# Optimization experiments

Measured on AMD Instinct MI355X. Metric: run time of the kernel, lower is better.

The kernel has to match this reference:

```python
import jax, jax.numpy as jnp
import numpy as np

N, E, DIN, HID, HEADS = 50000, 400000, 256, 64, 4
EPS_BN = 1e-5

def setup_inputs() -> dict:
    key = jax.random.key(0)
    ks = jax.random.split(key, 12)
    inp = {}
    inp['x'] = jax.random.normal(ks[0], (N, DIN), dtype=jnp.float32)
    inp['edge_index'] = jax.random.randint(ks[1], (2, E), 0, N, dtype=jnp.int64)
    s = 1.0 / np.sqrt(DIN)
    inp['W1'] = jax.random.uniform(ks[2], (DIN, HEADS * HID), jnp.float32, -s, s)
    inp['a_src1'] = jax.random.normal(ks[3], (HEADS, HID), dtype=jnp.float32) * 0.1
    inp['a_dst1'] = jax.random.normal(ks[4], (HEADS, HID), dtype=jnp.float32) * 0.1
    inp['b1'] = jnp.zeros((HEADS * HID,), jnp.float32)
    inp['bn1_w'] = jnp.ones((HEADS * HID,), jnp.float32)
    inp['bn1_b'] = jnp.zeros((HEADS * HID,), jnp.float32)
    inp['bn1_m'] = jnp.zeros((HEADS * HID,), jnp.float32)
    inp['bn1_v'] = jnp.ones((HEADS * HID,), jnp.float32)
    s2 = 1.0 / np.sqrt(HEADS * HID)
    inp['W2'] = jax.random.uniform(ks[5], (HEADS * HID, HID), jnp.float32, -s2, s2)
    inp['a_src2'] = jax.random.normal(ks[6], (1, HID), dtype=jnp.float32) * 0.1
    inp['a_dst2'] = jax.random.normal(ks[7], (1, HID), dtype=jnp.float32) * 0.1
    inp['b2'] = jnp.zeros((HID,), jnp.float32)
    inp['bn2_w'] = jnp.ones((HID,), jnp.float32)
    inp['bn2_b'] = jnp.zeros((HID,), jnp.float32)
    inp['bn2_m'] = jnp.zeros((HID,), jnp.float32)
    inp['bn2_v'] = jnp.ones((HID,), jnp.float32)
    sr = 1.0 / np.sqrt(HID)
    inp['Wr'] = jax.random.uniform(ks[8], (HID, 1), jnp.float32, -sr, sr)
    inp['br'] = jnp.zeros((1,), jnp.float32)
    inp['Wc'] = jax.random.uniform(ks[9], (HID, 1), jnp.float32, -sr, sr)
    inp['bc'] = jnp.zeros((1,), jnp.float32)
    return inp

def gat_layer(x, src, dst, W, a_src, a_dst, bias, concat):
    # x: [N, Fin] -> h: [N, H, D]
    H, D = a_src.shape
    h = (x @ W).reshape(-1, H, D)
    alpha_s = jnp.sum(h * a_src[None], axis=-1)  # [N, H]
    alpha_d = jnp.sum(h * a_dst[None], axis=-1)
    e = jax.nn.leaky_relu(alpha_s[src] + alpha_d[dst], 0.2)  # [Et, H]
    m = jax.ops.segment_max(e, dst, num_segments=N)
    m = jnp.where(jnp.isfinite(m), m, 0.0)
    ex = jnp.exp(e - m[dst])
    denom = jax.ops.segment_sum(ex, dst, num_segments=N)
    alpha = ex / (denom[dst] + 1e-16)  # segment softmax over incoming edges
    msg = h[src] * alpha[:, :, None]  # [Et, H, D]
    out = jax.ops.segment_sum(msg, dst, num_segments=N)  # [N, H, D]
    out = out.reshape(N, H * D) if concat else out.mean(axis=1)
    return out + bias

def batchnorm(x, w, b, mean, var):
    return (x - mean) * jax.lax.rsqrt(var + EPS_BN) * w + b

def reference(x, edge_index, W1, a_src1, a_dst1, b1, bn1_w, bn1_b, bn1_m, bn1_v,
              W2, a_src2, a_dst2, b2, bn2_w, bn2_b, bn2_m, bn2_v, Wr, br, Wc, bc):
    # add self loops (PyG GATConv default)
    loops = jnp.arange(N, dtype=edge_index.dtype)
    src = jnp.concatenate([edge_index[0], loops])
    dst = jnp.concatenate([edge_index[1], loops])
    h = gat_layer(x, src, dst, W1, a_src1, a_dst1, b1, concat=True)
    h = jax.nn.elu(batchnorm(h, bn1_w, bn1_b, bn1_m, bn1_v))
    h = gat_layer(h, src, dst, W2, a_src2, a_dst2, b2, concat=False)
    h = jax.nn.elu(batchnorm(h, bn2_w, bn2_b, bn2_m, bn2_v))
    reg = h @ Wr + br
    clf = jax.nn.sigmoid(h @ Wc + bc)
    return reg, clf
```

## Files before the change

kernel.cpp:

```cpp
#include <hip/hip_runtime.h>
#include <math.h>


typedef unsigned short ushort_t;
typedef unsigned char uchar_t;
typedef __attribute__((ext_vector_type(8))) unsigned short ushort8;
typedef __attribute__((ext_vector_type(4))) unsigned short ushort4v;
typedef __attribute__((ext_vector_type(8))) short short8;
typedef __attribute__((ext_vector_type(4))) float f32x4;
typedef __attribute__((ext_vector_type(2))) float f32x2;

#define EPS_BN 1e-5f

__device__ __forceinline__ ushort_t f2bf(float f) {
  unsigned u = __float_as_uint(f);
  unsigned r = u + 0x7fffu + ((u >> 16) & 1u);
  return (ushort_t)(r >> 16);
}
__device__ __forceinline__ float bf2f(ushort_t h) {
  return __uint_as_float((unsigned)h << 16);
}
__device__ __forceinline__ uchar_t f2fp8(float f) {
  return (uchar_t)(__builtin_amdgcn_cvt_pk_fp8_f32(f, f, 0, false) & 0xff);
}
__device__ __forceinline__ float leaky02(float x) { return x >= 0.f ? x : 0.2f * x; }
__device__ __forceinline__ float elu_fast(float x) {
  return x > 0.f ? x : __expf(x) - 1.f;
}
__device__ __forceinline__ float wave_sum(float v) {
#pragma unroll
  for (int o = 1; o < 64; o <<= 1) v += __shfl_xor(v, o, 64);
  return v;
}
__device__ __forceinline__ int wave_incl_scan(int v, int lane) {
#pragma unroll
  for (int off = 1; off < 64; off <<= 1) {
    int t = __shfl_up(v, off, 64);
    if (lane >= off) v += t;
  }
  return v;
}

__device__ __forceinline__ void gld_lds16(const ushort_t* g, ushort_t* l) {
  __builtin_amdgcn_global_load_lds(
      (const __attribute__((address_space(1))) unsigned int*)g,
      (__attribute__((address_space(3))) unsigned int*)l, 16, 0, 0);
}

__global__ __launch_bounds__(256) void hist_kernel(
    const int* __restrict__ dst, int* __restrict__ counts, int E) {
  int e = blockIdx.x * blockDim.x + threadIdx.x;
  if (e < E) atomicAdd(&counts[dst[e]], 1);
}

__global__ __launch_bounds__(256) void scan_chunks_kernel(
    const int* __restrict__ counts, int* __restrict__ offsets, int* __restrict__ partials,
    int N, int E, int* __restrict__ csr_src,
    const float* __restrict__ W1, const float* __restrict__ W2,
    ushort_t* __restrict__ W1t, ushort_t* __restrict__ W2t,
    const float* __restrict__ b1, const float* __restrict__ bn1w,
    const float* __restrict__ bn1b, const float* __restrict__ bn1m,
    const float* __restrict__ bn1v,
    const float* __restrict__ b2, const float* __restrict__ bn2w,
    const float* __restrict__ bn2b, const float* __restrict__ bn2m,
    const float* __restrict__ bn2v,
    float* __restrict__ S1, float* __restrict__ T1,
    float* __restrict__ S2, float* __restrict__ T2) {
  __shared__ int ws[4];
  const int tid = threadIdx.x, lane = tid & 63, wv = tid >> 6;
  const int i = blockIdx.x * 256 + tid;
  const int gsz = gridDim.x * 256;
  int v = (i < N) ? counts[i] : 0;
  int incl = wave_incl_scan(v, lane);
  if (lane == 63) ws[wv] = incl;
  __syncthreads();
  int wbase = 0;
  for (int k = 0; k < wv; ++k) wbase += ws[k];
  if (i < N) offsets[i] = wbase + incl - v;
  if (tid == 255) partials[blockIdx.x] = wbase + incl;

  for (int j = i; j < 256 * 256; j += gsz) {
    int k = j >> 8, n2 = j & 255;
    W1t[n2 * 256 + k] = f2bf(W1[j]);
  }
  for (int j = i; j < 256 * 64; j += gsz) {
    int k = j >> 6, n2 = j & 63;
    W2t[n2 * 256 + k] = f2bf(W2[j]);
  }
  if (i < 256) {
    float s = bn1w[i] * rsqrtf(bn1v[i] + EPS_BN);
    S1[i] = s;
    T1[i] = (b1[i] - bn1m[i]) * s + bn1b[i];
  } else if (i < 320) {
    int j = i - 256;
    float s = bn2w[j] * rsqrtf(bn2v[j] + EPS_BN);
    S2[j] = s;
    T2[j] = (b2[j] - bn2m[j]) * s + bn2b[j];
  } else if (i < 384) {
    csr_src[E + i - 320] = 0;
  }
}

__global__ __launch_bounds__(256) void scatter_kernel(
    const int* __restrict__ src, const int* __restrict__ dst,
    const int* __restrict__ offsets, const int* __restrict__ partials,
    int* __restrict__ cursor, int* __restrict__ csr_src,
    int* __restrict__ offs2, int E, int N, int nb) {
  __shared__ int pp[256];
  __shared__ int ws[4];
  __shared__ int tot;
  const int tid = threadIdx.x, lane = tid & 63, wv = tid >> 6;
  int v = (tid < nb) ? partials[tid] : 0;
  int incl = wave_incl_scan(v, lane);
  if (lane == 63) ws[wv] = incl;
  __syncthreads();
  int wbase = 0;
  for (int k = 0; k < wv; ++k) wbase += ws[k];
  pp[tid] = wbase + incl - v;
  if (tid == 255) tot = wbase + incl;
  __syncthreads();

  int idx = blockIdx.x * 256 + tid;
  if (idx < E) {
    int d = dst[idx];
    int p = atomicAdd(&cursor[d], 1);
    csr_src[offsets[d] + pp[d >> 8] + p] = src[idx];
  }
  if (idx <= N) {
    offs2[idx] = (idx < N) ? offsets[idx] + pp[idx >> 8] : tot;
  }
}

__global__ __launch_bounds__(512) void gemm1_persist(
    const float* __restrict__ X, const ushort_t* __restrict__ Bt,
    uchar_t* __restrict__ Cout, const float* __restrict__ avs,
    const float* __restrict__ avd,
    float* __restrict__ as_out, float* __restrict__ ad_out, int M, int ntiles) {
  __shared__ ushort_t Bs[256 * 256];
  __shared__ ushort_t As[32 * 256];
  const int t = threadIdx.x;
  const int w = t >> 6, l = t & 63;
  const int wr = w >> 2, wc = w & 3;

#pragma unroll
  for (int it = 0; it < 16; ++it) {
    int s = it * 512 + t;
    int i = s >> 5, sr = s & 31;
    int kb = sr >> 3, sl8 = sr & 7;
    int kc = (sl8 ^ (i & 7)) << 3;
    gld_lds16(Bt + (size_t)i * 256 + kb * 64 + kc, &Bs[s * 8]);
  }

  const int ar = t >> 4, k0a = (t & 15) * 16;
  int wd0, wd1;
  {
    int k = k0a;
    wd0 = ar * 256 + (k & ~63) + ((k & 63) ^ ((ar & 7) << 3));
    k = k0a + 8;
    wd1 = ar * 256 + (k & ~63) + ((k & 63) ^ ((ar & 7) << 3));
  }
  float4 fa0, fa1, fa2, fa3;
  {
    const float* src = X + (size_t)min(blockIdx.x * 32 + ar, M - 1) * 256 + k0a;
    fa0 = *(const float4*)(src);
    fa1 = *(const float4*)(src + 4);
    fa2 = *(const float4*)(src + 8);
    fa3 = *(const float4*)(src + 12);
  }

  const int fr = l & 15;
  const int kq = (l >> 4) << 3;
  const int fx = (fr & 7) << 3;
  const ushort_t* Ab = &As[(wr * 16 + fr) << 8];
  const ushort_t* Bb = &Bs[(wc * 64 + fr) << 8];

  float asw[4], adw[4];
#pragma unroll
  for (int j = 0; j < 4; ++j) {
    asw[j] = avs[wc * 64 + fr + j * 16];
    adw[j] = avd[wc * 64 + fr + j * 16];
  }

  for (int tile = blockIdx.x; tile < ntiles; tile += 256) {
    ushort8 u0, u1;
    u0[0] = f2bf(fa0.x); u0[1] = f2bf(fa0.y); u0[2] = f2bf(fa0.z); u0[3] = f2bf(fa0.w);
    u0[4] = f2bf(fa1.x); u0[5] = f2bf(fa1.y); u0[6] = f2bf(fa1.z); u0[7] = f2bf(fa1.w);
    u1[0] = f2bf(fa2.x); u1[1] = f2bf(fa2.y); u1[2] = f2bf(fa2.z); u1[3] = f2bf(fa2.w);
    u1[4] = f2bf(fa3.x); u1[5] = f2bf(fa3.y); u1[6] = f2bf(fa3.z); u1[7] = f2bf(fa3.w);
    __syncthreads();
    *(ushort8*)&As[wd0] = u0;
    *(ushort8*)&As[wd1] = u1;
    __syncthreads();

    {
      int nt_ = tile + 256;
      if (nt_ < ntiles) {
        const float* src = X + (size_t)min(nt_ * 32 + ar, M - 1) * 256 + k0a;
        fa0 = *(const float4*)(src);
        fa1 = *(const float4*)(src + 4);
        fa2 = *(const float4*)(src + 8);
        fa3 = *(const float4*)(src + 12);
      }
    }

    f32x4 acc[4];
#pragma unroll
    for (int j = 0; j < 4; ++j) acc[j] = (f32x4){0.f, 0.f, 0.f, 0.f};
#pragma unroll
    for (int k0 = 0; k0 < 256; k0 += 32) {
      const int kabs = k0 + kq;
      const int base = (kabs & ~63) + ((kabs & 63) ^ fx);
      short8 af = *(const short8*)&Ab[base];
#pragma unroll
      for (int j = 0; j < 4; ++j) {
        short8 bf8 = *(const short8*)&Bb[j * 4096 + base];
        acc[j] = __builtin_amdgcn_mfma_f32_16x16x32_bf16(af, bf8, acc[j], 0, 0, 0);
      }
    }

    const int rbase = tile * 32 + wr * 16 + (l >> 4) * 4;
#pragma unroll
    for (int j = 0; j < 4; ++j)
#pragma unroll
      for (int r4 = 0; r4 < 4; ++r4) {
        int row = rbase + r4;
        if (row < M)
          Cout[(size_t)row * 256 + wc * 64 + fr + j * 16] = f2fp8(acc[j][r4]);
      }

#pragma unroll
    for (int r4 = 0; r4 < 4; ++r4) {
      float s_ = acc[0][r4] * asw[0] + acc[1][r4] * asw[1] +
                 acc[2][r4] * asw[2] + acc[3][r4] * asw[3];
      float d_ = acc[0][r4] * adw[0] + acc[1][r4] * adw[1] +
                 acc[2][r4] * adw[2] + acc[3][r4] * adw[3];
#pragma unroll
      for (int o = 1; o < 16; o <<= 1) {
        s_ += __shfl_xor(s_, o, 64);
        d_ += __shfl_xor(d_, o, 64);
      }
      if ((l & 15) == 0) {
        int row = rbase + r4;
        if (row < M) {
          as_out[(size_t)row * 4 + wc] = s_;
          ad_out[(size_t)row * 4 + wc] = d_;
        }
      }
    }
  }
}

__global__ __launch_bounds__(256) void gemm2_fullk(
    const ushort_t* __restrict__ Ain, const ushort_t* __restrict__ Bt,
    ushort_t* __restrict__ Cout, const float* __restrict__ avs,
    const float* __restrict__ avd,
    float* __restrict__ as_out, float* __restrict__ ad_out, int M) {
  __shared__ ushort_t As[64 * 256];
  __shared__ ushort_t Bs[64 * 256];
  const int t = threadIdx.x;
  const int w = t >> 6, l = t & 63;
  const int m0 = blockIdx.x * 64;

  {
    const int slot = l & 7;
#pragma unroll
    for (int i = 0; i < 8; ++i) {
      const int r = w * 64 + i * 8 + (l >> 3);
      const int ir = r >> 2, kb = r & 3;
      const int kc = (slot ^ (ir & 7)) << 3;
      gld_lds16(Bt + (size_t)ir * 256 + kb * 64 + kc, &Bs[w * 4096 + i * 512]);
    }
#pragma unroll
    for (int i = 0; i < 8; ++i) {
      const int r = w * 64 + i * 8 + (l >> 3);
      const int ir = r >> 2, kb = r & 3;
      const int kc = (slot ^ (ir & 7)) << 3;
      const int arow = min(m0 + ir, M - 1);
      gld_lds16(Ain + (size_t)arow * 256 + kb * 64 + kc, &As[w * 4096 + i * 512]);
    }
  }
  asm volatile("s_waitcnt vmcnt(8)" ::: "memory");
  __builtin_amdgcn_s_barrier();
  asm volatile("s_waitcnt vmcnt(0)" ::: "memory");
  __builtin_amdgcn_sched_barrier(0);

  f32x4 acc[4];
#pragma unroll
  for (int j = 0; j < 4; ++j) acc[j] = (f32x4){0.f, 0.f, 0.f, 0.f};

  const int fr = l & 15;
  const int kq = (l >> 4) << 3;
  const int fx = (fr & 7) << 3;
  const ushort_t* Ab = &As[(w * 16 + fr) << 8];
  const ushort_t* Bb = &Bs[fr << 8];
#pragma unroll
  for (int k0 = 0; k0 < 256; k0 += 32) {
    const int kabs = k0 + kq;
    const int base = (kabs & ~63) + ((kabs & 63) ^ fx);
    short8 af = *(const short8*)&Ab[base];
#pragma unroll
    for (int j = 0; j < 4; ++j) {
      short8 bf8 = *(const short8*)&Bb[j * 4096 + base];
      acc[j] = __builtin_amdgcn_mfma_f32_16x16x32_bf16(af, bf8, acc[j], 0, 0, 0);
    }
  }

  const int rbase = m0 + w * 16 + (l >> 4) * 4;
#pragma unroll
  for (int j = 0; j < 4; ++j)
#pragma unroll
    for (int r4 = 0; r4 < 4; ++r4) {
      int row = rbase + r4;
      if (row < M)
        Cout[(size_t)row * 64 + fr + j * 16] = f2bf(acc[j][r4]);
    }

  float asw[4], adw[4];
#pragma unroll
  for (int j = 0; j < 4; ++j) {
    asw[j] = avs[fr + j * 16];
    adw[j] = avd[fr + j * 16];
  }
#pragma unroll
  for (int r4 = 0; r4 < 4; ++r4) {
    float s_ = acc[0][r4] * asw[0] + acc[1][r4] * asw[1] +
               acc[2][r4] * asw[2] + acc[3][r4] * asw[3];
    float d_ = acc[0][r4] * adw[0] + acc[1][r4] * adw[1] +
               acc[2][r4] * adw[2] + acc[3][r4] * adw[3];
#pragma unroll
    for (int o = 1; o < 16; o <<= 1) {
      s_ += __shfl_xor(s_, o, 64);
      d_ += __shfl_xor(d_, o, 64);
    }
    if ((l & 15) == 0) {
      int row = rbase + r4;
      if (row < M) {
        as_out[row] = s_;
        ad_out[row] = d_;
      }
    }
  }
}

__global__ __launch_bounds__(256) void agg1_kernel(
    const uchar_t* __restrict__ h1, const int* __restrict__ offsets,
    const int* __restrict__ csr, const float* __restrict__ as1,
    const float* __restrict__ ad1,
    const float* __restrict__ S1, const float* __restrict__ T1,
    ushort_t* __restrict__ out, int N) {
  __shared__ int ldsS[4][64];
  __shared__ float ldsW[4][64][4];
  const int wv = threadIdx.x >> 6;
  const int l = threadIdx.x & 63;
  const int h = l >> 5, q = l & 31;
  const int hb = h << 5;
  const int hh = q >> 3;
  int n = blockIdx.x * 8 + wv * 2 + h;
  const bool valid = (n < N);
  if (!valid) n = N - 1;
  const int off = offsets[n], deg = offsets[n + 1] - off;
  const int* csrp = csr + off;
  const unsigned fb = (unsigned)q << 3;
  float4 adn = *(const float4*)&ad1[n * 4];
  const int degw = max(deg, __shfl_xor(deg, 32, 64));

  f32x2 a0 = {0.f, 0.f}, a1 = {0.f, 0.f}, a2 = {0.f, 0.f}, a3 = {0.f, 0.f};
  float den = 0.f;

  for (int base = 0; base < degw; base += 32) {
    int s = 0;
    float4 w4 = make_float4(0.f, 0.f, 0.f, 0.f);
    int idx = base + q;
    if (idx < deg) {
      s = csrp[idx];
      float4 a4 = *(const float4*)&as1[s * 4];
      w4.x = __expf(leaky02(a4.x + adn.x));
      w4.y = __expf(leaky02(a4.y + adn.y));
      w4.z = __expf(leaky02(a4.z + adn.z));
      w4.w = __expf(leaky02(a4.w + adn.w));
    }
    ldsS[wv][l] = s;
    *(float4*)&ldsW[wv][l][0] = w4;
    int cntw = min(32, degw - base);
    for (int j = 0; j < cntw; j += 8) {
#pragma unroll
      for (int i = 0; i < 8; ++i) {
        int e = j + i;
        int se = ldsS[wv][hb + e];
        float we = ldsW[wv][hb + e][hh];
        uint2 d = *(const uint2*)&h1[(size_t)se * 256 + fb];
        f32x2 lo0 = __builtin_amdgcn_cvt_pk_f32_fp8(d.x, false);
        f32x2 hi0 = __builtin_amdgcn_cvt_pk_f32_fp8(d.x, true);
        f32x2 lo1 = __builtin_amdgcn_cvt_pk_f32_fp8(d.y, false);
        f32x2 hi1 = __builtin_amdgcn_cvt_pk_f32_fp8(d.y, true);
        f32x2 w2 = {we, we};
        a0 = lo0 * w2 + a0;
        a1 = hi0 * w2 + a1;
        a2 = lo1 * w2 + a2;
        a3 = hi1 * w2 + a3;
        den += we;
      }
    }
  }

  float ad_h = (hh & 2) ? ((hh & 1) ? adn.w : adn.z) : ((hh & 1) ? adn.y : adn.x);
  float4 asn = *(const float4*)&as1[n * 4];
  float as_h = (hh & 2) ? ((hh & 1) ? asn.w : asn.z) : ((hh & 1) ? asn.y : asn.x);
  float ws = __expf(leaky02(as_h + ad_h));
  {
    uint2 d = *(const uint2*)&h1[(size_t)n * 256 + fb];
    f32x2 lo0 = __builtin_amdgcn_cvt_pk_f32_fp8(d.x, false);
    f32x2 hi0 = __builtin_amdgcn_cvt_pk_f32_fp8(d.x, true);
    f32x2 lo1 = __builtin_amdgcn_cvt_pk_f32_fp8(d.y, false);
    f32x2 hi1 = __builtin_amdgcn_cvt_pk_f32_fp8(d.y, true);
    f32x2 w2 = {ws, ws};
    a0 = lo0 * w2 + a0;
    a1 = hi0 * w2 + a1;
    a2 = lo1 * w2 + a2;
    a3 = hi1 * w2 + a3;
  }
  float inv = 1.f / (den + ws + 1e-16f);

  const int c0 = q << 3;
  float4 Sv0 = *(const float4*)&S1[c0];
  float4 Sv1 = *(const float4*)&S1[c0 + 4];
  float4 Tv0 = *(const float4*)&T1[c0];
  float4 Tv1 = *(const float4*)&T1[c0 + 4];
  ushort8 o;
  o[0] = f2bf(elu_fast(fmaf(a0.x, inv * Sv0.x, Tv0.x)));
  o[1] = f2bf(elu_fast(fmaf(a0.y, inv * Sv0.y, Tv0.y)));
  o[2] = f2bf(elu_fast(fmaf(a1.x, inv * Sv0.z, Tv0.z)));
  o[3] = f2bf(elu_fast(fmaf(a1.y, inv * Sv0.w, Tv0.w)));
  o[4] = f2bf(elu_fast(fmaf(a2.x, inv * Sv1.x, Tv1.x)));
  o[5] = f2bf(elu_fast(fmaf(a2.y, inv * Sv1.y, Tv1.y)));
  o[6] = f2bf(elu_fast(fmaf(a3.x, inv * Sv1.z, Tv1.z)));
  o[7] = f2bf(elu_fast(fmaf(a3.y, inv * Sv1.w, Tv1.w)));
  if (valid) *(ushort8*)&out[(size_t)n * 256 + c0] = o;
}

__global__ __launch_bounds__(256) void agg2_kernel(
    const ushort_t* __restrict__ h2, const int* __restrict__ offsets,
    const int* __restrict__ csr, const float* __restrict__ as2,
    const float* __restrict__ ad2,
    const float* __restrict__ S2, const float* __restrict__ T2,
    const float* __restrict__ Wr, const float* __restrict__ br,
    const float* __restrict__ Wc, const float* __restrict__ bc,
    float* __restrict__ out_reg, float* __restrict__ out_clf, int N) {
  __shared__ float2 ldsSW[4][64];
  const int wv = threadIdx.x >> 6;
  const int l = threadIdx.x & 63;
  const int h = l >> 5, q = l & 31;
  int n = blockIdx.x * 8 + wv * 2 + h;
  const bool valid = (n < N);
  if (!valid) n = N - 1;
  const int off = offsets[n], deg = offsets[n + 1] - off;
  const int* csrp = csr + off;
  const float adn = ad2[n];
  const int degw = max(deg, __shfl_xor(deg, 32, 64));

  f32x2 acc = {0.f, 0.f};
  float den = 0.f;
  const int hb = h << 5;

  for (int base = 0; base < degw; base += 32) {
    int s = 0;
    float w_ = 0.f;
    int idx = base + q;
    if (idx < deg) {
      s = csrp[idx];
      w_ = __expf(leaky02(as2[s] + adn));
    }
    float2 sw;
    sw.x = __int_as_float(s);
    sw.y = w_;
    ldsSW[wv][l] = sw;
    int cntw = min(32, degw - base);
    for (int j = 0; j < cntw; j += 8) {
#pragma unroll
      for (int i = 0; i < 8; ++i) {
        int e = j + i;
        float2 t = ldsSW[wv][hb + e];
        int se = __float_as_int(t.x);
        float we = t.y;
        unsigned d = *(const unsigned*)&h2[(size_t)se * 64 + (q << 1)];
        acc.x = fmaf(we, bf2f((ushort_t)d), acc.x);
        acc.y = fmaf(we, bf2f((ushort_t)(d >> 16)), acc.y);
        den += we;
      }
    }
  }

  float ws = __expf(leaky02(as2[n] + adn));
  {
    unsigned d = *(const unsigned*)&h2[(size_t)n * 64 + (q << 1)];
    acc.x = fmaf(ws, bf2f((ushort_t)d), acc.x);
    acc.y = fmaf(ws, bf2f((ushort_t)(d >> 16)), acc.y);
  }
  float inv = 1.f / (den + ws + 1e-16f);

  const int c0 = q << 1;
  float2 Sv = *(const float2*)&S2[c0];
  float2 Tv = *(const float2*)&T2[c0];
  float2 wr = *(const float2*)&Wr[c0];
  float2 wc = *(const float2*)&Wc[c0];
  float o0 = elu_fast(fmaf(acc.x, inv * Sv.x, Tv.x));
  float o1 = elu_fast(fmaf(acc.y, inv * Sv.y, Tv.y));
  float rs = o0 * wr.x + o1 * wr.y;
  float cs = o0 * wc.x + o1 * wc.y;
#pragma unroll
  for (int o = 1; o < 32; o <<= 1) {
    rs += __shfl_xor(rs, o, 64);
    cs += __shfl_xor(cs, o, 64);
  }
  if (q == 0 && valid) {
    out_reg[n] = rs + br[0];
    float z = cs + bc[0];
    out_clf[n] = 1.f / (1.f + __expf(-z));
  }
}

extern "C" void kernel_launch(void* const* d_in, const int* in_sizes, int n_in,
                              void* d_out, int out_size, void* d_ws, size_t ws_size,
                              hipStream_t stream) {
  const float* x      = (const float*)d_in[0];
  const int*   ei     = (const int*)d_in[1];
  const float* W1     = (const float*)d_in[2];
  const float* a_src1 = (const float*)d_in[3];
  const float* a_dst1 = (const float*)d_in[4];
  const float* b1     = (const float*)d_in[5];
  const float* bn1w   = (const float*)d_in[6];
  const float* bn1b   = (const float*)d_in[7];
  const float* bn1m   = (const float*)d_in[8];
  const float* bn1v   = (const float*)d_in[9];
  const float* W2     = (const float*)d_in[10];
  const float* a_src2 = (const float*)d_in[11];
  const float* a_dst2 = (const float*)d_in[12];
  const float* b2     = (const float*)d_in[13];
  const float* bn2w   = (const float*)d_in[14];
  const float* bn2b   = (const float*)d_in[15];
  const float* bn2m   = (const float*)d_in[16];
  const float* bn2v   = (const float*)d_in[17];
  const float* Wr     = (const float*)d_in[18];
  const float* br     = (const float*)d_in[19];
  const float* Wc     = (const float*)d_in[20];
  const float* bc     = (const float*)d_in[21];

  const int N = in_sizes[0] / 256;
  const int E = in_sizes[1] / 2;
  const int* srcv = ei;
  const int* dstv = ei + E;

  char* w = (char*)d_ws;
  auto alloc = [&](size_t bytes) {
    char* p = w;
    w += (bytes + 255) & ~(size_t)255;
    return p;
  };
  const int nb = (N + 255) / 256;
  const size_t nbytes_rounded = ((size_t)N * 4 + 255) & ~(size_t)255;
  int* counts    = (int*)alloc((size_t)N * 4);
  int* cursor    = (int*)alloc((size_t)N * 4);
  int* offsets   = (int*)alloc((size_t)N * 4);
  int* offs2     = (int*)alloc((size_t)(N + 1) * 4);
  int* partials  = (int*)alloc((size_t)nb * 4);
  int* csr_src   = (int*)alloc((size_t)(E + 64) * 4);
  float* as1     = (float*)alloc((size_t)N * 4 * 4);
  float* ad1     = (float*)alloc((size_t)N * 4 * 4);
  float* as2     = (float*)alloc((size_t)N * 4);
  float* ad2     = (float*)alloc((size_t)N * 4);
  float* S1      = (float*)alloc(256 * 4);
  float* T1      = (float*)alloc(256 * 4);
  float* S2      = (float*)alloc(64 * 4);
  float* T2      = (float*)alloc(64 * 4);
  ushort_t* W1t  = (ushort_t*)alloc((size_t)256 * 256 * 2);
  ushort_t* W2t  = (ushort_t*)alloc((size_t)64 * 256 * 2);
  uchar_t* h1b   = (uchar_t*)alloc((size_t)N * 256);
  ushort_t* h1a  = (ushort_t*)alloc((size_t)N * 256 * 2);
  ushort_t* h2b  = (ushort_t*)alloc((size_t)N * 64 * 2);

  float* out_reg = (float*)d_out;

  hipMemsetAsync(counts, 0, nbytes_rounded * 2, stream);
  hist_kernel<<<(E + 255) / 256, 256, 0, stream>>>(dstv, counts, E);
  scan_chunks_kernel<<<nb, 256, 0, stream>>>(counts, offsets, partials, N, E, csr_src,
                                             W1, W2, W1t, W2t,
                                             b1, bn1w, bn1b, bn1m, bn1v,
                                             b2, bn2w, bn2b, bn2m, bn2v,
                                             S1, T1, S2, T2);
  {
    int items = max(E, N + 1);
    scatter_kernel<<<(items + 255) / 256, 256, 0, stream>>>(srcv, dstv, offsets, partials,
                                                            cursor, csr_src, offs2, E, N, nb);
  }

  const int nwb8 = (N + 7) / 8;
  const int ntiles1 = (N + 31) / 32;
  const int mtiles2 = (N + 63) / 64;

  gemm1_persist<<<256, 512, 0, stream>>>(
      x, W1t, h1b, a_src1, a_dst1, as1, ad1, N, ntiles1);
  agg1_kernel<<<nwb8, 256, 0, stream>>>(h1b, offs2, csr_src, as1, ad1, S1, T1, h1a, N);

  gemm2_fullk<<<mtiles2, 256, 0, stream>>>(
      h1a, W2t, h2b, a_src2, a_dst2, as2, ad2, N);
  agg2_kernel<<<nwb8, 256, 0, stream>>>(h2b, offs2, csr_src, as2, ad2, S2, T2,
                                        Wr, br, Wc, bc, out_reg, out_reg + N, N);
}
```

Before: 243.9 us.

## Fuse layer-1 aggregation with layer-2 GEMM through shared memory

Merges agg1_kernel and gemm2_fullk into one kernel. Each 512-thread block aggregates 16 nodes, writes the bf16 post-BN/ELU rows into a swizzled LDS tile, then one wave runs MFMA against W2 held in LDS and emits h2 plus the attention scores. This removes the N×256 bf16 intermediate's write and reread and one kernel launch. In exchange every block reloads the 32KB W2 tile into LDS, only one of eight waves does the GEMM, and LDS use per block grows, which may lower occupancy of the gather-bound aggregation.

Result: no change. 245.7 us (+0.8%).

```diff
diff --git a/kernel.cpp b/kernel.cpp
--- a/kernel.cpp
+++ b/kernel.cpp
@@ -250,114 +250,38 @@
   }
 }
 
-__global__ __launch_bounds__(256) void gemm2_fullk(
-    const ushort_t* __restrict__ Ain, const ushort_t* __restrict__ Bt,
-    ushort_t* __restrict__ Cout, const float* __restrict__ avs,
-    const float* __restrict__ avd,
-    float* __restrict__ as_out, float* __restrict__ ad_out, int M) {
-  __shared__ ushort_t As[64 * 256];
-  __shared__ ushort_t Bs[64 * 256];
-  const int t = threadIdx.x;
-  const int w = t >> 6, l = t & 63;
-  const int m0 = blockIdx.x * 64;
-
-  {
-    const int slot = l & 7;
-#pragma unroll
-    for (int i = 0; i < 8; ++i) {
-      const int r = w * 64 + i * 8 + (l >> 3);
-      const int ir = r >> 2, kb = r & 3;
-      const int kc = (slot ^ (ir & 7)) << 3;
-      gld_lds16(Bt + (size_t)ir * 256 + kb * 64 + kc, &Bs[w * 4096 + i * 512]);
-    }
-#pragma unroll
-    for (int i = 0; i < 8; ++i) {
-      const int r = w * 64 + i * 8 + (l >> 3);
-      const int ir = r >> 2, kb = r & 3;
-      const int kc = (slot ^ (ir & 7)) << 3;
-      const int arow = min(m0 + ir, M - 1);
-      gld_lds16(Ain + (size_t)arow * 256 + kb * 64 + kc, &As[w * 4096 + i * 512]);
-    }
-  }
-  asm volatile("s_waitcnt vmcnt(8)" ::: "memory");
-  __builtin_amdgcn_s_barrier();
-  asm volatile("s_waitcnt vmcnt(0)" ::: "memory");
-  __builtin_amdgcn_sched_barrier(0);
-
-  f32x4 acc[4];
-#pragma unroll
-  for (int j = 0; j < 4; ++j) acc[j] = (f32x4){0.f, 0.f, 0.f, 0.f};
-
-  const int fr = l & 15;
-  const int kq = (l >> 4) << 3;
-  const int fx = (fr & 7) << 3;
-  const ushort_t* Ab = &As[(w * 16 + fr) << 8];
-  const ushort_t* Bb = &Bs[fr << 8];
-#pragma unroll
-  for (int k0 = 0; k0 < 256; k0 += 32) {
-    const int kabs = k0 + kq;
-    const int base = (kabs & ~63) + ((kabs & 63) ^ fx);
-    short8 af = *(const short8*)&Ab[base];
-#pragma unroll
-    for (int j = 0; j < 4; ++j) {
-      short8 bf8 = *(const short8*)&Bb[j * 4096 + base];
-      acc[j] = __builtin_amdgcn_mfma_f32_16x16x32_bf16(af, bf8, acc[j], 0, 0, 0);
-    }
-  }
-
-  const int rbase = m0 + w * 16 + (l >> 4) * 4;
-#pragma unroll
-  for (int j = 0; j < 4; ++j)
-#pragma unroll
-    for (int r4 = 0; r4 < 4; ++r4) {
-      int row = rbase + r4;
-      if (row < M)
-        Cout[(size_t)row * 64 + fr + j * 16] = f2bf(acc[j][r4]);
-    }
-
-  float asw[4], adw[4];
-#pragma unroll
-  for (int j = 0; j < 4; ++j) {
-    asw[j] = avs[fr + j * 16];
-    adw[j] = avd[fr + j * 16];
-  }
-#pragma unroll
-  for (int r4 = 0; r4 < 4; ++r4) {
-    float s_ = acc[0][r4] * asw[0] + acc[1][r4] * asw[1] +
-               acc[2][r4] * asw[2] + acc[3][r4] * asw[3];
-    float d_ = acc[0][r4] * adw[0] + acc[1][r4] * adw[1] +
-               acc[2][r4] * adw[2] + acc[3][r4] * adw[3];
-#pragma unroll
-    for (int o = 1; o < 16; o <<= 1) {
-      s_ += __shfl_xor(s_, o, 64);
-      d_ += __shfl_xor(d_, o, 64);
-    }
-    if ((l & 15) == 0) {
-      int row = rbase + r4;
-      if (row < M) {
-        as_out[row] = s_;
-        ad_out[row] = d_;
-      }
-    }
-  }
-}
-
-__global__ __launch_bounds__(256) void agg1_kernel(
+__global__ __launch_bounds__(512) void agg1g2_kernel(
     const uchar_t* __restrict__ h1, const int* __restrict__ offsets,
     const int* __restrict__ csr, const float* __restrict__ as1,
     const float* __restrict__ ad1,
     const float* __restrict__ S1, const float* __restrict__ T1,
-    ushort_t* __restrict__ out, int N) {
-  __shared__ int ldsS[4][64];
-  __shared__ float ldsW[4][64][4];
-  const int wv = threadIdx.x >> 6;
-  const int l = threadIdx.x & 63;
+    const ushort_t* __restrict__ W2t,
+    const float* __restrict__ avs2, const float* __restrict__ avd2,
+    ushort_t* __restrict__ h2b, float* __restrict__ as2,
+    float* __restrict__ ad2, int N) {
+  __shared__ ushort_t Bs2[64 * 256];
+  __shared__ ushort_t As2[16 * 256];
+  __shared__ int ldsS[8][64];
+  __shared__ float ldsW[8][64][4];
+  const int t = threadIdx.x;
+  const int wv = t >> 6, l = t & 63;
   const int h = l >> 5, q = l & 31;
   const int hb = h << 5;
   const int hh = q >> 3;
-  int n = blockIdx.x * 8 + wv * 2 + h;
+  const int nloc = wv * 2 + h;
+  int n = blockIdx.x * 16 + nloc;
   const bool valid = (n < N);
   if (!valid) n = N - 1;
+
+#pragma unroll
+  for (int it = 0; it < 4; ++it) {
+    int s = it * 512 + t;
+    int i = s >> 5, sr = s & 31;
+    int kb = sr >> 3, sl8 = sr & 7;
+    int kc = (sl8 ^ (i & 7)) << 3;
+    gld_lds16(W2t + (size_t)i * 256 + kb * 64 + kc, &Bs2[s * 8]);
+  }
+
   const int off = offsets[n], deg = offsets[n + 1] - off;
   const int* csrp = csr + off;
   const unsigned fb = (unsigned)q << 3;
@@ -421,21 +345,83 @@
   }
   float inv = 1.f / (den + ws + 1e-16f);
 
-  const int c0 = q << 3;
-  float4 Sv0 = *(const float4*)&S1[c0];
-  float4 Sv1 = *(const float4*)&S1[c0 + 4];
-  float4 Tv0 = *(const float4*)&T1[c0];
-  float4 Tv1 = *(const float4*)&T1[c0 + 4];
-  ushort8 o;
-  o[0] = f2bf(elu_fast(fmaf(a0.x, inv * Sv0.x, Tv0.x)));
-  o[1] = f2bf(elu_fast(fmaf(a0.y, inv * Sv0.y, Tv0.y)));
-  o[2] = f2bf(elu_fast(fmaf(a1.x, inv * Sv0.z, Tv0.z)));
-  o[3] = f2bf(elu_fast(fmaf(a1.y, inv * Sv0.w, Tv0.w)));
-  o[4] = f2bf(elu_fast(fmaf(a2.x, inv * Sv1.x, Tv1.x)));
-  o[5] = f2bf(elu_fast(fmaf(a2.y, inv * Sv1.y, Tv1.y)));
-  o[6] = f2bf(elu_fast(fmaf(a3.x, inv * Sv1.z, Tv1.z)));
-  o[7] = f2bf(elu_fast(fmaf(a3.y, inv * Sv1.w, Tv1.w)));
-  if (valid) *(ushort8*)&out[(size_t)n * 256 + c0] = o;
+  {
+    const int c0 = q << 3;
+    float4 Sv0 = *(const float4*)&S1[c0];
+    float4 Sv1 = *(const float4*)&S1[c0 + 4];
+    float4 Tv0 = *(const float4*)&T1[c0];
+    float4 Tv1 = *(const float4*)&T1[c0 + 4];
+    ushort8 o;
+    o[0] = f2bf(elu_fast(fmaf(a0.x, inv * Sv0.x, Tv0.x)));
+    o[1] = f2bf(elu_fast(fmaf(a0.y, inv * Sv0.y, Tv0.y)));
+    o[2] = f2bf(elu_fast(fmaf(a1.x, inv * Sv0.z, Tv0.z)));
+    o[3] = f2bf(elu_fast(fmaf(a1.y, inv * Sv0.w, Tv0.w)));
+    o[4] = f2bf(elu_fast(fmaf(a2.x, inv * Sv1.x, Tv1.x)));
+    o[5] = f2bf(elu_fast(fmaf(a2.y, inv * Sv1.y, Tv1.y)));
+    o[6] = f2bf(elu_fast(fmaf(a3.x, inv * Sv1.z, Tv1.z)));
+    o[7] = f2bf(elu_fast(fmaf(a3.y, inv * Sv1.w, Tv1.w)));
+    const int dst = nloc * 256 + ((q >> 3) << 6) + (((q & 7) ^ (nloc & 7)) << 3);
+    *(ushort8*)&As2[dst] = o;
+  }
+  __syncthreads();
+
+  if (wv == 0) {
+    f32x4 acc[4];
+#pragma unroll
+    for (int j = 0; j < 4; ++j) acc[j] = (f32x4){0.f, 0.f, 0.f, 0.f};
+    const int fr = l & 15;
+    const int kq = (l >> 4) << 3;
+    const int fx = (fr & 7) << 3;
+    const ushort_t* Ab = &As2[fr << 8];
+    const ushort_t* Bb = &Bs2[fr << 8];
+#pragma unroll
+    for (int k0 = 0; k0 < 256; k0 += 32) {
+      const int kabs = k0 + kq;
+      const int base = (kabs & ~63) + ((kabs & 63) ^ fx);
+      short8 af = *(const short8*)&Ab[base];
+#pragma unroll
+      for (int j = 0; j < 4; ++j) {
+        short8 bf8 = *(const short8*)&Bb[j * 4096 + base];
+        acc[j] = __builtin_amdgcn_mfma_f32_16x16x32_bf16(af, bf8, acc[j], 0, 0, 0);
+      }
+    }
+
+    const int rbase = blockIdx.x * 16 + (l >> 4) * 4;
+#pragma unroll
+    for (int j = 0; j < 4; ++j)
+#pragma unroll
+      for (int r4 = 0; r4 < 4; ++r4) {
+        int row = rbase + r4;
+        if (row < N)
+          h2b[(size_t)row * 64 + fr + j * 16] = f2bf(acc[j][r4]);
+      }
+
+    float asw[4], adw[4];
+#pragma unroll
+    for (int j = 0; j < 4; ++j) {
+      asw[j] = avs2[fr + j * 16];
+      adw[j] = avd2[fr + j * 16];
+    }
+#pragma unroll
+    for (int r4 = 0; r4 < 4; ++r4) {
+      float s_ = acc[0][r4] * asw[0] + acc[1][r4] * asw[1] +
+                 acc[2][r4] * asw[2] + acc[3][r4] * asw[3];
+      float d_ = acc[0][r4] * adw[0] + acc[1][r4] * adw[1] +
+                 acc[2][r4] * adw[2] + acc[3][r4] * adw[3];
+#pragma unroll
+      for (int o = 1; o < 16; o <<= 1) {
+        s_ += __shfl_xor(s_, o, 64);
+        d_ += __shfl_xor(d_, o, 64);
+      }
+      if ((l & 15) == 0) {
+        int row = rbase + r4;
+        if (row < N) {
+          as2[row] = s_;
+          ad2[row] = d_;
+        }
+      }
+    }
+  }
 }
 
 __global__ __launch_bounds__(256) void agg2_kernel(
@@ -575,7 +561,6 @@
   ushort_t* W1t  = (ushort_t*)alloc((size_t)256 * 256 * 2);
   ushort_t* W2t  = (ushort_t*)alloc((size_t)64 * 256 * 2);
   uchar_t* h1b   = (uchar_t*)alloc((size_t)N * 256);
-  ushort_t* h1a  = (ushort_t*)alloc((size_t)N * 256 * 2);
   ushort_t* h2b  = (ushort_t*)alloc((size_t)N * 64 * 2);
 
   float* out_reg = (float*)d_out;
@@ -595,14 +580,15 @@
 
   const int nwb8 = (N + 7) / 8;
   const int ntiles1 = (N + 31) / 32;
-  const int mtiles2 = (N + 63) / 64;
+  const int nblk16 = (N + 15) / 16;
 
   gemm1_persist<<<256, 512, 0, stream>>>(
       x, W1t, h1b, a_src1, a_dst1, as1, ad1, N, ntiles1);
-  agg1_kernel<<<nwb8, 256, 0, stream>>>(h1b, offs2, csr_src, as1, ad1, S1, T1, h1a, N);
-
-  gemm2_fullk<<<mtiles2, 256, 0, stream>>>(
-      h1a, W2t, h2b, a_src2, a_dst2, as2, ad2, N);
+
+  agg1g2_kernel<<<nblk16, 512, 0, stream>>>(
+      h1b, offs2, csr_src, as1, ad1, S1, T1, W2t, a_src2, a_dst2,
+      h2b, as2, ad2, N);
+
   agg2_kernel<<<nwb8, 256, 0, stream>>>(h2b, offs2, csr_src, as2, ad2, S2, T2,
                                         Wr, br, Wc, bc, out_reg, out_reg + N, N);
 }
```
